# Kernel tuning notes

Hardware: AMD Instinct MI355X
Metric: run time of the kernel (lower is better)

Reference implementation:

```python
import jax, jax.numpy as jnp
import numpy as np

NUM_LEVELS = 2
RADIUS = 3


def setup_inputs() -> dict:
    key = jax.random.key(0)
    k1, k2, k3 = jax.random.split(key, 3)
    x = jax.random.normal(k1, (4, 320, 9, 32, 32), dtype=jnp.float32)
    w_fc0 = jax.random.normal(k2, (160, 320), dtype=jnp.float32) * 0.05
    w_fc1 = jax.random.normal(k3, (160, 320), dtype=jnp.float32) * 0.05
    return {"x": x, "w_fc0": w_fc0, "w_fc1": w_fc1}


def _bilinear_zeros(img, xs, ys):
    # img: (M, H, W); xs, ys: (M, K) pixel coords.
    # Matches F.grid_sample(mode='bilinear', padding_mode='zeros', align_corners=True):
    # align_corners normalization round-trips to the raw pixel coords, and
    # out-of-bounds corners contribute zero.
    M, H, W = img.shape
    x0f = jnp.floor(xs)
    y0f = jnp.floor(ys)
    wx = xs - x0f
    wy = ys - y0f
    x0 = x0f.astype(jnp.int32)
    y0 = y0f.astype(jnp.int32)
    x1 = x0 + 1
    y1 = y0 + 1
    n = jnp.arange(M)[:, None]

    def corner(yi, xi):
        valid = (xi >= 0) & (xi < W) & (yi >= 0) & (yi < H)
        v = img[n, jnp.clip(yi, 0, H - 1), jnp.clip(xi, 0, W - 1)]
        return v * valid.astype(img.dtype)

    v00 = corner(y0, x0)
    v01 = corner(y0, x1)
    v10 = corner(y1, x0)
    v11 = corner(y1, x1)
    return (v00 * (1 - wx) * (1 - wy) + v01 * wx * (1 - wy)
            + v10 * (1 - wx) * wy + v11 * wx * wy)


def reference(x, w_fc0, w_fc1):
    b, c, T, h, w = x.shape
    xt = jnp.transpose(x, (0, 2, 1, 3, 4))  # (b, T, c, h, w)
    # 1x1 convs (no bias) on consecutive-frame pairs
    f0 = jnp.einsum('btchw,oc->bothw', xt[:, :-1], w_fc0)
    f1 = jnp.einsum('btchw,oc->bothw', xt[:, 1:], w_fc1)
    t = T - 1
    c2 = w_fc0.shape[0]
    f0 = f0.reshape(b * t, c2, h * w)
    f1 = f1.reshape(b * t, c2, h * w)
    # all-pairs correlation volume, normalized by channel count
    corr = jnp.einsum('nci,ncj->nij', f0, f1) / c2  # (bt, hw, hw)
    corr = corr.reshape(b * t * h * w, h, w)

    # pyramid via 2x2 avg pooling
    pyramid = [corr]
    for _ in range(NUM_LEVELS - 1):
        M, H, W = pyramid[-1].shape
        pyramid.append(pyramid[-1].reshape(M, H // 2, 2, W // 2, 2).mean(axis=(2, 4)))

    # per-pixel centroids (x, y), tiled over the bt batch axis
    ys, xs = jnp.meshgrid(jnp.arange(h), jnp.arange(w), indexing='ij')
    cx = jnp.tile(xs.reshape(-1).astype(jnp.float32), b * t)  # (bt*h*w,)
    cy = jnp.tile(ys.reshape(-1).astype(jnp.float32), b * t)

    # delta[i, j] = (d[i], d[j]); delta[...,0] -> x offset, delta[...,1] -> y offset
    r = RADIUS
    d = jnp.linspace(-r, r, 2 * r + 1)
    dx = jnp.repeat(d, 2 * r + 1)  # varies along first window dim
    dy = jnp.tile(d, 2 * r + 1)    # varies along second window dim

    outs = []
    for i, ci in enumerate(pyramid):
        xs_s = cx[:, None] / (2 ** i) + dx[None, :]  # (M, K)
        ys_s = cy[:, None] / (2 ** i) + dy[None, :]
        v = _bilinear_zeros(ci, xs_s, ys_s)          # (M, (2r+1)^2)
        outs.append(v.reshape(b * t, h, w, -1))
    out = jnp.concatenate(outs, axis=3)              # (bt, h, w, L*(2r+1)^2)
    out = out.reshape(b, t, h, w, -1)
    return jnp.transpose(out, (0, 4, 1, 2, 3)).astype(jnp.float32)
```

## Files before the change

kernel.cpp:

```cpp
#include <hip/hip_runtime.h>
#include <hip/hip_bf16.h>

typedef __attribute__((ext_vector_type(8))) short short8;
typedef __attribute__((ext_vector_type(4))) float f32x4;

static constexpr int HW = 1024;
static constexpr int C2 = 160;
static constexpr int FS = 168;
static constexpr int FSC = 160;
static constexpr int KSTEPS = 10;
static constexpr int XST = 264;
static constexpr size_t PL = 32ull * 1024 * 160;
static constexpr size_t PPL = 32ull * 256 * 160;
static constexpr int AIMG = 6656;

__device__ inline short bfh(float v) {
  __hip_bfloat16 h = __float2bfloat16(v);
  return *reinterpret_cast<short*>(&h);
}
__device__ inline float bff(short s) {
  union { unsigned u; float f; } c;
  c.u = ((unsigned)(unsigned short)s) << 16;
  return c.f;
}

typedef const __attribute__((address_space(1))) void* gas_t;
typedef __attribute__((address_space(3))) void* las_t;
__device__ inline void gload_lds16(const void* g, void* l) {
  __builtin_amdgcn_global_load_lds((gas_t)g, (las_t)l, 16, 0, 0);
}

__global__ __launch_bounds__(256)
void wprep2_kernel(const float* __restrict__ w0, const float* __restrict__ w1,
                   short* __restrict__ wp) {
  const int id = blockIdx.x * 256 + threadIdx.x;
  if (id >= KSTEPS * 4 * AIMG) return;
  const int img = id / AIMG, r = id % AIMG;
  const int ks = img >> 2, qp = img & 3;
  short outv = 0;
  if (r < 6400) {
    const int hl = r / 3200;
    const int g2 = r % 3200;
    const int gr = g2 / 40, kk = g2 % 40;
    const int mat = gr >= 40;
    const int o = qp * 40 + gr - mat * 40;
    if (kk < 32) {
      const float v = (mat ? w1 : w0)[o * 320 + ks * 32 + kk];
      const short hb = bfh(v);
      outv = hl ? bfh(v - bff(hb)) : hb;
    }
  }
  wp[id] = outv;
}

__global__ __launch_bounds__(512)
void conv_fused(const float* __restrict__ x, const short* __restrict__ wprep2,
                short* __restrict__ f0bh, short* __restrict__ f0bl,
                short* __restrict__ f1bh, short* __restrict__ f1bl) {
  __shared__ __align__(16) char lds[51296];
  float* xF = reinterpret_cast<float*>(lds);
  short* aL = reinterpret_cast<short*>(lds + 37984);
  short* tL = reinterpret_cast<short*>(lds);

  const int pxt = blockIdx.x;
  const int qp = blockIdx.y;
  const int bb = blockIdx.z;
  const int tid = threadIdx.x;
  const int lane = tid & 63;
  const int wave = __builtin_amdgcn_readfirstlane(tid >> 6);
  const int lr = lane & 15, kg = lane >> 4;
  const int fgrp = wave >> 1;
  const int pxh = wave & 1;

  const int l8 = lane >> 3;
  const int l7 = lane & 7;
  const int px = pxh * 16 + lr;
  const int pxs = px ^ (kg << 3);

  f32x4 acc[5][3];
#pragma unroll
  for (int mt = 0; mt < 5; ++mt)
#pragma unroll
    for (int fi = 0; fi < 3; ++fi)
#pragma unroll
      for (int r = 0; r < 4; ++r) acc[mt][fi][r] = 0.f;

  const float* xg = x + ((size_t)(bb * 320) * 9) * 1024 + (size_t)pxt * 32;

  for (int ks = 0; ks < KSTEPS; ++ks) {
    if (ks) __syncthreads();
    {
      const short* asrc = wprep2 + (size_t)(ks * 4 + qp) * AIMG;
#pragma unroll
      for (int jj = 0; jj < 2; ++jj) {
        const int j = wave * 2 + jj;
        if (j < 13) gload_lds16(asrc + j * 512 + lane * 8, aL + j * 512);
      }
    }
#pragma unroll
    for (int jj = 0; jj < 5; ++jj) {
      const int gi = wave + jj * 8;
      if (gi < 36) {
        const int f = gi >> 2, oct = gi & 3;
        const int c = ks * 32 + oct * 8 + l8;
        const float* src =
            xg + ((size_t)c * 9 + f) * 1024 + ((l7 ^ (oct << 1)) << 2);
        gload_lds16(src, xF + gi * XST);
      }
    }
    __syncthreads();

    short8 Ah[5], Al[5];
#pragma unroll
    for (int mt = 0; mt < 5; ++mt) {
      Ah[mt] = *reinterpret_cast<const short8*>(&aL[(mt * 16 + lr) * 40 + kg * 8]);
      Al[mt] = *reinterpret_cast<const short8*>(&aL[3200 + (mt * 16 + lr) * 40 + kg * 8]);
    }
#pragma unroll
    for (int fi = 0; fi < 3; ++fi) {
      const int f = fgrp + fi * 4;
      if (f < 9) {
        const float* bp = xF + (f * 4 + kg) * XST + pxs;
        float xv[8];
#pragma unroll
        for (int j = 0; j < 8; ++j) xv[j] = bp[j * 32];
        short8 Bh, Bl;
#pragma unroll
        for (int j = 0; j < 8; ++j) {
          const short h = bfh(xv[j]);
          Bh[j] = h;
          Bl[j] = bfh(xv[j] - bff(h));
        }
#pragma unroll
        for (int mt = 0; mt < 5; ++mt) {
          acc[mt][fi] = __builtin_amdgcn_mfma_f32_16x16x32_bf16(Ah[mt], Bh, acc[mt][fi], 0, 0, 0);
          acc[mt][fi] = __builtin_amdgcn_mfma_f32_16x16x32_bf16(Ah[mt], Bl, acc[mt][fi], 0, 0, 0);
          acc[mt][fi] = __builtin_amdgcn_mfma_f32_16x16x32_bf16(Al[mt], Bh, acc[mt][fi], 0, 0, 0);
        }
      }
    }
  }

#pragma unroll
  for (int m = 0; m < 2; ++m) {
    __syncthreads();
#pragma unroll
    for (int mt = 0; mt < 5; ++mt)
#pragma unroll
      for (int fi = 0; fi < 3; ++fi) {
        const int f = fgrp + fi * 4;
        const int tt = f - m;
        if (f < 9 && (unsigned)tt < 8u) {
#pragma unroll
          for (int rr = 0; rr < 4; ++rr) {
            const int gr = mt * 16 + kg * 4 + rr;
            if ((gr >= 40) == (m == 1)) {
              const int rowl = gr - m * 40;
              const int ql = rowl / 20, r20 = rowl % 20;
              const int c = 8 * r20 + tt;
              const int row = ql * 32 + pxh * 16 + lr;
              const float v = acc[mt][fi][rr];
              const short h = bfh(v);
              tL[row * FS + c] = h;
              tL[10752 + row * FS + c] = bfh(v - bff(h));
            }
          }
        }
      }
    __syncthreads();
#pragma unroll
    for (int i = 0; i < 5; ++i) {
      const int idx = tid + i * 512;
      const int plane = idx / 1280, rem = idx % 1280;
      const int row = rem / 20, c16 = rem % 20;
      const int ql = row >> 5, pxl = row & 31;
      const int n = bb * 8 + qp * 2 + ql;
      short* dst = (m == 0) ? (plane ? f0bl : f0bh) : (plane ? f1bl : f1bh);
      *reinterpret_cast<uint4*>(dst + ((size_t)n * 1024 + pxt * 32 + pxl) * 160 + c16 * 8) =
          *reinterpret_cast<const uint4*>(&tL[plane * 10752 + row * FS + c16 * 8]);
    }
  }
}

__global__ __launch_bounds__(256)
void pool_b(const short* __restrict__ f1bh, const short* __restrict__ f1bl,
            short* __restrict__ g1pbh, short* __restrict__ g1pbl) {
  const int id = blockIdx.x * 256 + threadIdx.x;
  if (id >= 32 * 256 * 20) return;
  const int c16 = id % 20;
  const int PX = (id / 20) & 255;
  const int n = id / (20 * 256);
  const int Y = PX >> 4, X = PX & 15;
  const int r0 = Y * 64 + X * 2;
  const size_t base = ((size_t)n * 1024 + r0) * 160 + c16 * 8;
  const short8 h00 = *reinterpret_cast<const short8*>(f1bh + base);
  const short8 h01 = *reinterpret_cast<const short8*>(f1bh + base + 160);
  const short8 h10 = *reinterpret_cast<const short8*>(f1bh + base + 32 * 160);
  const short8 h11 = *reinterpret_cast<const short8*>(f1bh + base + 33 * 160);
  const short8 l00 = *reinterpret_cast<const short8*>(f1bl + base);
  const short8 l01 = *reinterpret_cast<const short8*>(f1bl + base + 160);
  const short8 l10 = *reinterpret_cast<const short8*>(f1bl + base + 32 * 160);
  const short8 l11 = *reinterpret_cast<const short8*>(f1bl + base + 33 * 160);
  short8 ho, lo;
#pragma unroll
  for (int j = 0; j < 8; ++j) {
    const float v = 0.25f * ((bff(h00[j]) + bff(l00[j])) + (bff(h01[j]) + bff(l01[j])) +
                             (bff(h10[j]) + bff(l10[j])) + (bff(h11[j]) + bff(l11[j])));
    const short h = bfh(v);
    ho[j] = h;
    lo[j] = bfh(v - bff(h));
  }
  const size_t ob = ((size_t)n * 256 + PX) * 160 + c16 * 8;
  *reinterpret_cast<short8*>(g1pbh + ob) = ho;
  *reinterpret_cast<short8*>(g1pbl + ob) = lo;
}

__global__ __launch_bounds__(256)
void corr_kernel(const short* __restrict__ f0bh, const short* __restrict__ f0bl,
                 const short* __restrict__ f1bh, const short* __restrict__ f1bl,
                 const short* __restrict__ g1pbh, const short* __restrict__ g1pbl,
                 float* __restrict__ out) {
  __shared__ __align__(16) short f0L[2][32 * FSC];
  __shared__ __align__(16) short f1L[2][32 * FSC];
  __shared__ float S0[32 * 33];
  __shared__ float S1[2][32 * 17];
  const int flat = blockIdx.x;
  const int xcd = flat & 7;
  const int rr_ = flat >> 3;
  const int y = rr_ & 31;
  const int n = (xcd << 2) | (rr_ >> 5);
  const int bb = n >> 3, q = n & 7;
  const int tid = threadIdx.x;
  const int lane = tid & 63;
  const int wave = __builtin_amdgcn_readfirstlane(tid >> 6);
  const int lr = lane & 15, kg = lane >> 4;
  const int xx = tid & 31;
  const int hi = tid >> 5;
  const float inv = 1.f / 160.f;
  const size_t obase = (size_t)(bb * 784 + q) * 1024 + (size_t)y * 32;

  {
    const short* s0 = f0bh + ((size_t)n * 1024 + y * 32) * 160;
    const short* s1 = f0bl + ((size_t)n * 1024 + y * 32) * 160;
#pragma unroll
    for (int jj = 0; jj < 5; ++jj) {
      const int j = wave * 5 + jj;
      const int pl = j / 10, off = (j % 10) * 512;
      gload_lds16((pl ? s1 : s0) + off + lane * 8, &f0L[pl][off]);
    }
  }
  __syncthreads();

  const int mi0 = wave >> 1, ni0 = wave & 1;
  short8 a0h[5], a0l[5];
#pragma unroll
  for (int ks = 0; ks < 5; ++ks) {
    a0h[ks] = *reinterpret_cast<const short8*>(&f0L[0][(mi0 * 16 + lr) * FSC + ks * 32 + kg * 8]);
    a0l[ks] = *reinterpret_cast<const short8*>(&f0L[1][(mi0 * 16 + lr) * FSC + ks * 32 + kg * 8]);
  }

  for (int dyi = 0; dyi < 7; ++dyi) {
    const int yy = y + dyi - 3;
    const bool inr = (unsigned)yy < 32u;
    __syncthreads();
    if (inr) {
      const short* s0 = f1bh + ((size_t)n * 1024 + yy * 32) * 160;
      const short* s1 = f1bl + ((size_t)n * 1024 + yy * 32) * 160;
#pragma unroll
      for (int jj = 0; jj < 5; ++jj) {
        const int j = wave * 5 + jj;
        const int pl = j / 10, off = (j % 10) * 512;
        gload_lds16((pl ? s1 : s0) + off + lane * 8, &f1L[pl][off]);
      }
    }
    __syncthreads();
    if (inr) {
      f32x4 aA = {0.f, 0.f, 0.f, 0.f}, aB = aA, aC = aA;
#pragma unroll
      for (int ks = 0; ks < 5; ++ks) {
        const short8 bh = *reinterpret_cast<const short8*>(&f1L[0][(ni0 * 16 + lr) * FSC + ks * 32 + kg * 8]);
        const short8 bl = *reinterpret_cast<const short8*>(&f1L[1][(ni0 * 16 + lr) * FSC + ks * 32 + kg * 8]);
        aA = __builtin_amdgcn_mfma_f32_16x16x32_bf16(a0h[ks], bh, aA, 0, 0, 0);
        aB = __builtin_amdgcn_mfma_f32_16x16x32_bf16(a0h[ks], bl, aB, 0, 0, 0);
        aC = __builtin_amdgcn_mfma_f32_16x16x32_bf16(a0l[ks], bh, aC, 0, 0, 0);
      }
#pragma unroll
      for (int r = 0; r < 4; ++r)
        S0[(mi0 * 16 + kg * 4 + r) * 33 + ni0 * 16 + lr] = (aA[r] + aB[r]) + aC[r];
    }
    __syncthreads();
    if (hi < 7) {
      const int x2 = xx + hi - 3;
      const float val = (inr && (unsigned)x2 < 32u) ? S0[xx * 33 + x2] * inv : 0.f;
      out[obase + (size_t)(hi * 7 + dyi) * 8192 + xx] = val;
    }
  }

  short8 a1h[5], a1l[5];
  if (wave < 2) {
#pragma unroll
    for (int ks = 0; ks < 5; ++ks) {
      a1h[ks] = *reinterpret_cast<const short8*>(&f0L[0][(wave * 16 + lr) * FSC + ks * 32 + kg * 8]);
      a1l[ks] = *reinterpret_cast<const short8*>(&f0L[1][(wave * 16 + lr) * FSC + ks * 32 + kg * 8]);
    }
  }
  const int Y0 = (y >> 1) - 3;
  const float wy = (y & 1) ? 0.5f : 0.f;
  for (int v = 0; v < 8; ++v) {
    const int Y = Y0 + v;
    const bool inr = (unsigned)Y < 16u;
    __syncthreads();
    if (inr) {
      const short* s0 = g1pbh + ((size_t)n * 256 + Y * 16) * 160;
      const short* s1 = g1pbl + ((size_t)n * 256 + Y * 16) * 160;
#pragma unroll
      for (int jj = 0; jj < 3; ++jj) {
        const int j = wave * 3 + jj;
        if (j < 10) {
          const int pl = j / 5, off = (j % 5) * 512;
          gload_lds16((pl ? s1 : s0) + off + lane * 8, &f1L[pl][off]);
        }
      }
    }
    __syncthreads();
    if (wave < 2) {
      f32x4 aA = {0.f, 0.f, 0.f, 0.f}, aB = aA, aC = aA;
      if (inr) {
#pragma unroll
        for (int ks = 0; ks < 5; ++ks) {
          const short8 bh = *reinterpret_cast<const short8*>(&f1L[0][lr * FSC + ks * 32 + kg * 8]);
          const short8 bl = *reinterpret_cast<const short8*>(&f1L[1][lr * FSC + ks * 32 + kg * 8]);
          aA = __builtin_amdgcn_mfma_f32_16x16x32_bf16(a1h[ks], bh, aA, 0, 0, 0);
          aB = __builtin_amdgcn_mfma_f32_16x16x32_bf16(a1h[ks], bl, aB, 0, 0, 0);
          aC = __builtin_amdgcn_mfma_f32_16x16x32_bf16(a1l[ks], bh, aC, 0, 0, 0);
        }
      }
#pragma unroll
      for (int r = 0; r < 4; ++r)
        S1[v & 1][(wave * 16 + kg * 4 + r) * 17 + lr] = (aA[r] + aB[r]) + aC[r];
    }
    __syncthreads();
    if (v >= 1 && hi < 7) {
      const int dyi = v - 1;
      const int Xl = (xx >> 1) - 3 + hi;
      const int Xr = Xl + 1;
      const float* t0 = S1[(v - 1) & 1];
      const float* t1 = S1[v & 1];
      const float a00 = ((unsigned)Xl < 16u) ? t0[xx * 17 + Xl] : 0.f;
      const float a01 = ((unsigned)Xr < 16u) ? t0[xx * 17 + Xr] : 0.f;
      const float a10 = ((unsigned)Xl < 16u) ? t1[xx * 17 + Xl] : 0.f;
      const float a11 = ((unsigned)Xr < 16u) ? t1[xx * 17 + Xr] : 0.f;
      const float wx = (xx & 1) ? 0.5f : 0.f;
      const float val = ((1.f - wx) * ((1.f - wy) * a00 + wy * a10) +
                         wx * ((1.f - wy) * a01 + wy * a11)) * inv;
      out[obase + (size_t)(49 + hi * 7 + dyi) * 8192 + xx] = val;
    }
  }
}

extern "C" void kernel_launch(void* const* d_in, const int* in_sizes, int n_in,
                              void* d_out, int out_size, void* d_ws,
                              size_t ws_size, hipStream_t stream) {
  const float* x = (const float*)d_in[0];
  const float* w0 = (const float*)d_in[1];
  const float* w1 = (const float*)d_in[2];
  short* f0bh = (short*)d_ws;
  short* f0bl = f0bh + PL;
  short* f1bh = f0bl + PL;
  short* f1bl = f1bh + PL;
  short* g1pbh = f1bl + PL;
  short* g1pbl = g1pbh + PPL;
  short* wprep2 = g1pbh;
  float* out = (float*)d_out;

  wprep2_kernel<<<1040, 256, 0, stream>>>(w0, w1, wprep2);
  conv_fused<<<dim3(32, 4, 4), 512, 0, stream>>>(x, wprep2, f0bh, f0bl, f1bh, f1bl);
  pool_b<<<640, 256, 0, stream>>>(f1bh, f1bl, g1pbh, g1pbl);
  corr_kernel<<<1024, 256, 0, stream>>>(f0bh, f0bl, f1bh, f1bl, g1pbh, g1pbl, out);
}
```

Baseline: 76.62 us.

## Double-buffer conv LDS loads to overlap next k-step fetch with MFMA

Doubles the LDS staging for weights and input tiles and issues the global-to-LDS loads for the next k-step before computing the current one. Per-wave vmcnt waits plus raw s_barrier replace the full __syncthreads pair, so memory latency can overlap with the MFMA work. The cost is doubling LDS use to about 100KB per block, which lowers occupancy, and the hand-counted vmcnt values must match the number of loads each wave issues.

```diff
diff --git a/kernel.cpp b/kernel.cpp
--- a/kernel.cpp
+++ b/kernel.cpp
@@ -10,6 +10,7 @@
 static constexpr int FSC = 160;
 static constexpr int KSTEPS = 10;
 static constexpr int XST = 264;
+static constexpr int XBUF = 9504;
 static constexpr size_t PL = 32ull * 1024 * 160;
 static constexpr size_t PPL = 32ull * 256 * 160;
 static constexpr int AIMG = 6656;
@@ -57,9 +58,9 @@
 void conv_fused(const float* __restrict__ x, const short* __restrict__ wprep2,
                 short* __restrict__ f0bh, short* __restrict__ f0bl,
                 short* __restrict__ f1bh, short* __restrict__ f1bl) {
-  __shared__ __align__(16) char lds[51296];
+  __shared__ __align__(16) char lds[102656];
   float* xF = reinterpret_cast<float*>(lds);
-  short* aL = reinterpret_cast<short*>(lds + 37984);
+  short* aL = reinterpret_cast<short*>(lds + 76032);
   short* tL = reinterpret_cast<short*>(lds);
 
   const int pxt = blockIdx.x;
@@ -87,40 +88,55 @@
 
   const float* xg = x + ((size_t)(bb * 320) * 9) * 1024 + (size_t)pxt * 32;
 
+#define ISSUE(KS, BUF)                                                        \
+  {                                                                           \
+    const short* asrc = wprep2 + (size_t)((KS) * 4 + qp) * AIMG;              \
+    _Pragma("unroll") for (int jj = 0; jj < 2; ++jj) {                        \
+      const int j = wave * 2 + jj;                                            \
+      if (j < 13)                                                             \
+        gload_lds16(asrc + j * 512 + lane * 8, aL + (BUF) * AIMG + j * 512);  \
+    }                                                                         \
+    _Pragma("unroll") for (int jj = 0; jj < 5; ++jj) {                        \
+      const int gi = wave + jj * 8;                                           \
+      if (gi < 36) {                                                          \
+        const int f_ = gi >> 2, oct_ = gi & 3;                                \
+        const int c_ = (KS) * 32 + oct_ * 8 + l8;                             \
+        gload_lds16(xg + ((size_t)c_ * 9 + f_) * 1024 + ((l7 ^ (oct_ << 1)) << 2), \
+                    xF + (BUF) * XBUF + gi * XST);                            \
+      }                                                                       \
+    }                                                                         \
+  }
+
+  ISSUE(0, 0);
+
+#pragma unroll
   for (int ks = 0; ks < KSTEPS; ++ks) {
-    if (ks) __syncthreads();
-    {
-      const short* asrc = wprep2 + (size_t)(ks * 4 + qp) * AIMG;
-#pragma unroll
-      for (int jj = 0; jj < 2; ++jj) {
-        const int j = wave * 2 + jj;
-        if (j < 13) gload_lds16(asrc + j * 512 + lane * 8, aL + j * 512);
-      }
-    }
-#pragma unroll
-    for (int jj = 0; jj < 5; ++jj) {
-      const int gi = wave + jj * 8;
-      if (gi < 36) {
-        const int f = gi >> 2, oct = gi & 3;
-        const int c = ks * 32 + oct * 8 + l8;
-        const float* src =
-            xg + ((size_t)c * 9 + f) * 1024 + ((l7 ^ (oct << 1)) << 2);
-        gload_lds16(src, xF + gi * XST);
-      }
-    }
-    __syncthreads();
-
+    const int buf = ks & 1;
+    if (ks + 1 < KSTEPS) {
+      ISSUE(ks + 1, buf ^ 1);
+      if (wave < 4)       asm volatile("s_waitcnt vmcnt(7)" ::: "memory");
+      else if (wave < 6)  asm volatile("s_waitcnt vmcnt(6)" ::: "memory");
+      else if (wave == 6) asm volatile("s_waitcnt vmcnt(5)" ::: "memory");
+      else                asm volatile("s_waitcnt vmcnt(4)" ::: "memory");
+    } else {
+      asm volatile("s_waitcnt vmcnt(0)" ::: "memory");
+    }
+    __builtin_amdgcn_s_barrier();
+    __builtin_amdgcn_sched_barrier(0);
+
+    const short* aB = aL + buf * AIMG;
+    const float* xB = xF + buf * XBUF;
     short8 Ah[5], Al[5];
 #pragma unroll
     for (int mt = 0; mt < 5; ++mt) {
-      Ah[mt] = *reinterpret_cast<const short8*>(&aL[(mt * 16 + lr) * 40 + kg * 8]);
-      Al[mt] = *reinterpret_cast<const short8*>(&aL[3200 + (mt * 16 + lr) * 40 + kg * 8]);
+      Ah[mt] = *reinterpret_cast<const short8*>(&aB[(mt * 16 + lr) * 40 + kg * 8]);
+      Al[mt] = *reinterpret_cast<const short8*>(&aB[3200 + (mt * 16 + lr) * 40 + kg * 8]);
     }
 #pragma unroll
     for (int fi = 0; fi < 3; ++fi) {
       const int f = fgrp + fi * 4;
       if (f < 9) {
-        const float* bp = xF + (f * 4 + kg) * XST + pxs;
+        const float* bp = xB + (f * 4 + kg) * XST + pxs;
         float xv[8];
 #pragma unroll
         for (int j = 0; j < 8; ++j) xv[j] = bp[j * 32];
@@ -139,7 +155,9 @@
         }
       }
     }
-  }
+    __builtin_amdgcn_s_barrier();
+  }
+#undef ISSUE
 
 #pragma unroll
   for (int m = 0; m < 2; ++m) {
```

New measurement: 85.49 us. +11.6%, slower.
